# Performance work log

Hardware: AMD Instinct MI355X
Metric: run time of the kernel (lower is better)

Reference implementation:

```python
import jax, jax.numpy as jnp
import numpy as np

FILTERS = 128
DN = ('NHWC', 'HWIO', 'NHWC')
T1 = 1.0
RTOL = 1e-3
ATOL = 1e-3
DT0 = 0.05
MAX_STEPS = 32  # upper bound on adaptive solver steps (dopri5 at rtol=1e-3 uses far fewer)


def _conv(x, w):
    return jax.lax.conv_general_dilated(x, w, (1, 1), 'SAME', dimension_numbers=DN)


def _ode_func(y, t, w1, b1, w2, b2):
    # f(y, t) = relu(conv(relu(conv([y, t], w1)+b1) ++ t, w2)+b2), time appended as extra channel
    def cat_t(x):
        return jnp.concatenate([x, jnp.ones(x.shape[:-1] + (1,), x.dtype) * t], axis=-1)
    h = jax.nn.relu(_conv(cat_t(y), w1) + b1)
    return jax.nn.relu(_conv(cat_t(h), w2) + b2)


def _dopri5(y0, w1, b1, w2, b2):
    # Adaptive Dormand-Prince RK45 from t=0 to t=1, matching tf.contrib.integrate.odeint defaults
    f = lambda y, t: _ode_func(y, t, w1, b1, w2, b2)

    def rk_step(y, t, dt):
        k1 = f(y, t)
        k2 = f(y + dt * (0.2 * k1), t + 0.2 * dt)
        k3 = f(y + dt * (3. / 40 * k1 + 9. / 40 * k2), t + 0.3 * dt)
        k4 = f(y + dt * (44. / 45 * k1 - 56. / 15 * k2 + 32. / 9 * k3), t + 0.8 * dt)
        k5 = f(y + dt * (19372. / 6561 * k1 - 25360. / 2187 * k2 + 64448. / 6561 * k3
                         - 212. / 729 * k4), t + 8. / 9 * dt)
        k6 = f(y + dt * (9017. / 3168 * k1 - 355. / 33 * k2 + 46732. / 5247 * k3
                         + 49. / 176 * k4 - 5103. / 18656 * k5), t + dt)
        y5 = y + dt * (35. / 384 * k1 + 500. / 1113 * k3 + 125. / 192 * k4
                       - 2187. / 6784 * k5 + 11. / 84 * k6)
        k7 = f(y5, t + dt)  # FSAL stage, used only for the error estimate here
        err = dt * ((35. / 384 - 5179. / 57600) * k1 + (500. / 1113 - 7571. / 16695) * k3
                    + (125. / 192 - 393. / 640) * k4 + (-2187. / 6784 + 92097. / 339200) * k5
                    + (11. / 84 - 187. / 2100) * k6 - (1. / 40) * k7)
        return y5, err

    def step(carry, _):
        y, t, dt, done = carry
        dt_c = jnp.minimum(dt, T1 - t)  # never overshoot t1
        y_new, err = rk_step(y, t, dt_c)
        scale = ATOL + RTOL * jnp.maximum(jnp.abs(y), jnp.abs(y_new))
        err_norm = jnp.sqrt(jnp.mean(jnp.square(err / scale)))
        err_norm = jax.lax.stop_gradient(jnp.maximum(err_norm, 1e-10))
        accept = err_norm <= 1.0
        factor = jnp.clip(0.9 * err_norm ** -0.2, 0.2, 10.0)
        adv = accept & jnp.logical_not(done)
        y = jnp.where(adv, y_new, y)
        t = jnp.where(adv, t + dt_c, t)
        dt = jnp.where(done, dt, dt_c * factor)
        done = done | (t >= T1 - 1e-6)
        return (y, t, dt, done), None

    init = (y0, jnp.float32(0.0), jnp.float32(DT0), jnp.array(False))
    (y, _, _, _), _ = jax.lax.scan(jax.checkpoint(step), init, None, length=MAX_STEPS)
    return y


def setup_inputs() -> dict:
    key = jax.random.key(0)
    k0, k1, k2 = jax.random.split(key, 3)
    B, H, W, F = 32, 32, 32, FILTERS
    kh = kw = 3
    # glorot_uniform for HWIO conv kernel: fan_in = kh*kw*(F+1), fan_out = kh*kw*F
    lim = float(np.sqrt(6.0 / (kh * kw * (F + 1) + kh * kw * F)))
    x = jax.random.normal(k0, (B, H, W, F), jnp.float32)
    w1 = jax.random.uniform(k1, (kh, kw, F + 1, F), jnp.float32, -lim, lim)
    w2 = jax.random.uniform(k2, (kh, kw, F + 1, F), jnp.float32, -lim, lim)
    b1 = jnp.zeros((F,), jnp.float32)
    b2 = jnp.zeros((F,), jnp.float32)
    return {"x": x, "w1": w1, "b1": b1, "w2": w2, "b2": b2}


def reference(x, w1, b1, w2, b2):
    return _dopri5(x, w1, b1, w2, b2)
```

## Files before the change

kernel.cpp:

```cpp
#include <hip/hip_runtime.h>
#include <math.h>

#define NB    32
#define NHW   32
#define NC    128
#define NTOT  (NB*NHW*NHW*NC)
#define N4    (NTOT/4)
#define N8    (NTOT/8)
#define KDIM  1152

typedef unsigned short u16;
typedef __attribute__((ext_vector_type(8))) short short8v;
typedef __attribute__((ext_vector_type(4))) float float4v;

__device__ inline float b2f(u16 u) { union { unsigned int i; float f; } x; x.i = ((unsigned int)u) << 16; return x.f; }
__device__ inline u16   f2b(float f) {
    union { unsigned int i; float f; } x; x.f = f;
    unsigned int u = x.i;
    return (u16)((u + 0x7fffu + ((u >> 16) & 1u)) >> 16);
}
__device__ inline void ld8(const u16* __restrict__ p, float* v) {
    uint4 r = *(const uint4*)p;
    v[0] = b2f((u16)(r.x & 0xffff)); v[1] = b2f((u16)(r.x >> 16));
    v[2] = b2f((u16)(r.y & 0xffff)); v[3] = b2f((u16)(r.y >> 16));
    v[4] = b2f((u16)(r.z & 0xffff)); v[5] = b2f((u16)(r.z >> 16));
    v[6] = b2f((u16)(r.w & 0xffff)); v[7] = b2f((u16)(r.w >> 16));
}
__device__ inline uint4 pk8(const float* v) {
    uint4 o;
    o.x = (unsigned int)f2b(v[0]) | ((unsigned int)f2b(v[1]) << 16);
    o.y = (unsigned int)f2b(v[2]) | ((unsigned int)f2b(v[3]) << 16);
    o.z = (unsigned int)f2b(v[4]) | ((unsigned int)f2b(v[5]) << 16);
    o.w = (unsigned int)f2b(v[6]) | ((unsigned int)f2b(v[7]) << 16);
    return o;
}
__device__ inline void fma8(float* __restrict__ v, const u16* __restrict__ p, float s) {
    float kv[8];
    ld8(p, kv);
    #pragma unroll
    for (int j = 0; j < 8; ++j) v[j] = fmaf(s, kv[j], v[j]);
}


__global__ __launch_bounds__(64) void init_kernel(float* __restrict__ st, double* __restrict__ acc)
{
    int i = threadIdx.x;
    if (i < 32) acc[i] = 0.0;
    if (i == 0) { st[0]=0.0f; st[1]=0.05f; st[2]=0.05f; st[3]=0.0f; st[4]=0.0f; }
}

__global__ __launch_bounds__(256) void prep_kernel(
    const float* __restrict__ w, short* __restrict__ Wt, float* __restrict__ Et)
{
    const int part = blockIdx.x;
    const int tid = threadIdx.x;
    if (part < 9) {
        const int tap = part;
        for (int i = tid; i < 128*128; i += 256) {
            const int ci = i >> 7, co = i & 127;
            Wt[co*KDIM + tap*128 + ci] = (short)f2b(w[(tap*129 + ci)*128 + co]);
        }
    } else {
        for (int i = tid; i < 9*128; i += 256) {
            const int cls = i >> 7, co = i & 127;
            const int cy = cls / 3, cx = cls % 3;
            float s = 0.f;
            for (int ky = 0; ky < 3; ++ky) {
                if ((cy==0 && ky==0) || (cy==2 && ky==2)) continue;
                for (int kx = 0; kx < 3; ++kx) {
                    if ((cx==0 && kx==0) || (cx==2 && kx==2)) continue;
                    s += w[((ky*3+kx)*129 + 128)*128 + co];
                }
            }
            Et[cls*128 + co] = s;
        }
    }
}

__global__ __launch_bounds__(256) void copy_kernel(float* __restrict__ dst, const float* __restrict__ src)
{
    int stride = gridDim.x * blockDim.x;
    for (int i = blockIdx.x*blockDim.x + threadIdx.x; i < N4; i += stride)
        reinterpret_cast<float4*>(dst)[i] = reinterpret_cast<const float4*>(src)[i];
}

__global__ __launch_bounds__(256) void copy_if_adv_kernel(float* __restrict__ dst,
                                                          const float* __restrict__ src,
                                                          const float* __restrict__ st)
{
    if (st[4] == 0.0f) return;
    int stride = gridDim.x * blockDim.x;
    for (int i = blockIdx.x*blockDim.x + threadIdx.x; i < N4; i += stride)
        reinterpret_cast<float4*>(dst)[i] = reinterpret_cast<const float4*>(src)[i];
}

template<int NK>
__global__ __launch_bounds__(256) void conv_mfma(
    const float* __restrict__ basef, const u16* __restrict__ bfin,
    const u16* __restrict__ ka, const u16* __restrict__ kb,
    const u16* __restrict__ kc, const u16* __restrict__ kd,
    const u16* __restrict__ ke,
    float ca, float cb, float cc2, float cd, float ce,
    const short* __restrict__ Wt, const float* __restrict__ bias,
    const float* __restrict__ Et,
    u16* __restrict__ out,
    const float* __restrict__ st, float cfrac)
{
    if (st[3] != 0.0f) return;
    __shared__ __align__(16) char lds[180*256];
    const int b    = blockIdx.y;
    const int tile = blockIdx.x;
    const int ty   = (tile >> 2) * 16;
    const int tx   = (tile & 3) * 8;
    const int tid  = threadIdx.x;
    const float dt = st[2];

    const size_t ibase = (size_t)b * (NHW*NHW*NC);
    for (int i = tid; i < 180*16; i += 256) {
        const int pos = i >> 4, cc = i & 15;
        const int sy = pos / 10, sx = pos - sy*10;
        const int gy = ty + sy - 1, gx = tx + sx - 1;
        const bool ok = ((unsigned)gy < 32u) && ((unsigned)gx < 32u);
        uint4 w128;
        if (!ok) {
            w128 = make_uint4(0u, 0u, 0u, 0u);
        } else if (NK < 0) {
            w128 = *(const uint4*)(bfin + ibase + (size_t)(gy*32 + gx)*128 + cc*8);
        } else {
            const size_t idx = ibase + (size_t)(gy*32 + gx)*128 + cc*8;
            float v[8];
            *(float4*)(v)     = *(const float4*)(basef + idx);
            *(float4*)(v + 4) = *(const float4*)(basef + idx + 4);
            if (NK >= 1) fma8(v, ka + idx, dt*ca);
            if (NK >= 2) fma8(v, kb + idx, dt*cb);
            if (NK >= 3) fma8(v, kc + idx, dt*cc2);
            if (NK >= 4) fma8(v, kd + idx, dt*cd);
            if (NK >= 5) fma8(v, ke + idx, dt*ce);
            w128 = pk8(v);
        }
        *(uint4*)(lds + pos*256 + ((cc*16) ^ ((pos & 7) << 4))) = w128;
    }
    __syncthreads();

    const int l  = tid & 63;
    const int w  = tid >> 6;
    const int wy = w >> 1, wx = w & 1;
    const int lr = l & 15,  kg = l >> 4;

    float4v acc[4][4];
    #pragma unroll
    for (int ra = 0; ra < 4; ++ra)
        #pragma unroll
        for (int nb = 0; nb < 4; ++nb)
            acc[ra][nb] = (float4v){0.f, 0.f, 0.f, 0.f};

    int sy0[4], sx0[4];
    #pragma unroll
    for (int ra = 0; ra < 4; ++ra) {
        const int r = wy*64 + ra*16 + lr;
        sy0[ra] = r >> 3; sx0[ra] = r & 7;
    }

    #pragma unroll
    for (int ky = 0; ky < 3; ++ky) {
        #pragma unroll
        for (int kx = 0; kx < 3; ++kx) {
            const int tap = ky*3 + kx;
            #pragma unroll
            for (int kk = 0; kk < 4; ++kk) {
                short8v a[4], bb[4];
                const int cc = kk*4 + kg;
                #pragma unroll
                for (int ra = 0; ra < 4; ++ra) {
                    const int pos = (sy0[ra] + ky)*10 + sx0[ra] + kx;
                    a[ra] = *(const short8v*)(lds + pos*256 + ((cc*16) ^ ((pos & 7) << 4)));
                }
                const short* wb = Wt + tap*128 + kk*32 + kg*8;
                #pragma unroll
                for (int nb = 0; nb < 4; ++nb) {
                    const int cout = wx*64 + nb*16 + lr;
                    bb[nb] = *(const short8v*)(wb + (size_t)cout*KDIM);
                }
                #pragma unroll
                for (int ra = 0; ra < 4; ++ra)
                    #pragma unroll
                    for (int nb = 0; nb < 4; ++nb)
                        acc[ra][nb] = __builtin_amdgcn_mfma_f32_16x16x32_bf16(a[ra], bb[nb], acc[ra][nb], 0, 0, 0);
            }
        }
    }

    const float tval = st[0] + cfrac*dt;
    #pragma unroll
    for (int nb = 0; nb < 4; ++nb) {
        const int cout = wx*64 + nb*16 + lr;
        const float bsv = bias[cout];
        #pragma unroll
        for (int ra = 0; ra < 4; ++ra) {
            #pragma unroll
            for (int ri = 0; ri < 4; ++ri) {
                const int r  = wy*64 + ra*16 + kg*4 + ri;
                const int yy = ty + (r >> 3), xx = tx + (r & 7);
                const int cy = (yy == 0) ? 0 : ((yy == 31) ? 2 : 1);
                const int cx = (xx == 0) ? 0 : ((xx == 31) ? 2 : 1);
                float v = acc[ra][nb][ri] + bsv + tval*Et[(cy*3 + cx)*128 + cout];
                v = fmaxf(v, 0.f);
                out[(size_t)b*131072 + (size_t)(yy*32 + xx)*128 + cout] = f2b(v);
            }
        }
    }
}

__global__ __launch_bounds__(256) void axpy5_kernel(
    float* __restrict__ y5, const float* __restrict__ y,
    const u16* __restrict__ k1, const u16* __restrict__ k3,
    const u16* __restrict__ k4, const u16* __restrict__ k5,
    const u16* __restrict__ k6,
    float c1, float c3, float c4, float c5, float c6,
    const float* __restrict__ st)
{
    if (st[3] != 0.0f) return;
    const float dt = st[2];
    int stride = gridDim.x * blockDim.x;
    for (int i = blockIdx.x*blockDim.x + threadIdx.x; i < N8; i += stride) {
        const size_t base = (size_t)i * 8;
        float v[8];
        *(float4*)(v)     = *(const float4*)(y + base);
        *(float4*)(v + 4) = *(const float4*)(y + base + 4);
        fma8(v, k1 + base, dt*c1);
        fma8(v, k3 + base, dt*c3);
        fma8(v, k4 + base, dt*c4);
        fma8(v, k5 + base, dt*c5);
        fma8(v, k6 + base, dt*c6);
        *(float4*)(y5 + base)     = *(const float4*)(v);
        *(float4*)(y5 + base + 4) = *(const float4*)(v + 4);
    }
}

__global__ __launch_bounds__(256) void err_reduce_kernel(
    const float* __restrict__ y,  const float* __restrict__ y5,
    const u16* __restrict__ k1, const u16* __restrict__ k3,
    const u16* __restrict__ k4, const u16* __restrict__ k5,
    const u16* __restrict__ k6, const u16* __restrict__ k7,
    const float* __restrict__ st, double* __restrict__ acc_slot)
{
    if (st[3] != 0.0f) return;
    const float dt = st[2];
    const float E1 = (float)(35.0/384.0 - 5179.0/57600.0);
    const float E3 = (float)(500.0/1113.0 - 7571.0/16695.0);
    const float E4 = (float)(125.0/192.0 - 393.0/640.0);
    const float E5 = (float)(-2187.0/6784.0 + 92097.0/339200.0);
    const float E6 = (float)(11.0/84.0 - 187.0/2100.0);
    const float E7 = (float)(-1.0/40.0);
    float lsum = 0.f;
    int stride = gridDim.x*blockDim.x;
    for (int i = blockIdx.x*blockDim.x + threadIdx.x; i < N8; i += stride) {
        const size_t base = (size_t)i * 8;
        float a[8], c[8], d[8], e[8], f[8], g[8], yv[8], v5[8];
        ld8(k1 + base, a); ld8(k3 + base, c); ld8(k4 + base, d);
        ld8(k5 + base, e); ld8(k6 + base, f); ld8(k7 + base, g);
        *(float4*)(yv)     = *(const float4*)(y + base);
        *(float4*)(yv + 4) = *(const float4*)(y + base + 4);
        *(float4*)(v5)     = *(const float4*)(y5 + base);
        *(float4*)(v5 + 4) = *(const float4*)(y5 + base + 4);
        #pragma unroll
        for (int j = 0; j < 8; ++j) {
            float err = dt*(E1*a[j] + E3*c[j] + E4*d[j] + E5*e[j] + E6*f[j] + E7*g[j]);
            float sc  = 1e-3f + 1e-3f*fmaxf(fabsf(yv[j]), fabsf(v5[j]));
            float r = err/sc; lsum += r*r;
        }
    }
    #pragma unroll
    for (int off = 32; off > 0; off >>= 1) lsum += __shfl_down(lsum, off, 64);
    __shared__ float ws_[4];
    int wid = threadIdx.x >> 6, lane = threadIdx.x & 63;
    if (lane == 0) ws_[wid] = lsum;
    __syncthreads();
    if (threadIdx.x == 0) {
        float bs = ws_[0] + ws_[1] + ws_[2] + ws_[3];
        atomicAdd(acc_slot, (double)bs);
    }
}

__global__ __launch_bounds__(64) void ctrl_kernel(float* __restrict__ st, const double* __restrict__ acc_slot)
{
    if (threadIdx.x != 0) return;
    float t = st[0], dt = st[1], dtc = st[2];
    bool done = (st[3] != 0.0f);
    float err_norm = sqrtf((float)(*acc_slot / (double)NTOT));
    err_norm = fmaxf(err_norm, 1e-10f);
    bool accept = (err_norm <= 1.0f);
    float factor = 0.9f * powf(err_norm, -0.2f);
    factor = fminf(fmaxf(factor, 0.2f), 10.0f);
    bool adv = accept && !done;
    if (adv) t = t + dtc;
    if (!done) dt = dtc * factor;
    done = done || (t >= 1.0f - 1e-6f);
    st[0] = t; st[1] = dt; st[3] = done ? 1.0f : 0.0f; st[4] = adv ? 1.0f : 0.0f;
    st[2] = fminf(dt, 1.0f - t);
}

extern "C" void kernel_launch(void* const* d_in, const int* in_sizes, int n_in,
                              void* d_out, int out_size, void* d_ws, size_t ws_size,
                              hipStream_t stream)
{
    const float* x  = (const float*)d_in[0];
    const float* w1 = (const float*)d_in[1];
    const float* b1 = (const float*)d_in[2];
    const float* w2 = (const float*)d_in[3];
    const float* b2 = (const float*)d_in[4];

    char* ws = (char*)d_ws;
    double* acc = (double*)ws;
    float*  st  = (float*)(ws + 256);
    float*  E1t = (float*)(ws + 512);
    float*  E2t = (float*)(ws + 5120);
    short*  Wt1 = (short*)(ws + 10240);
    short*  Wt2 = (short*)(ws + 10240 + 294912);
    char*   bufs = ws + 1048576;
    float* y  = (float*)(bufs);
    float* y5 = (float*)(bufs + (size_t)NTOT*4);
    u16*   h  = (u16*)(bufs + (size_t)NTOT*8);
    u16*   k1 = (u16*)(bufs + (size_t)NTOT*10);
    u16*   k2 = (u16*)(bufs + (size_t)NTOT*12);
    u16*   k3 = (u16*)(bufs + (size_t)NTOT*14);
    u16*   k4 = (u16*)(bufs + (size_t)NTOT*16);
    u16*   k5 = (u16*)(bufs + (size_t)NTOT*18);
    u16*   k6 = (u16*)(bufs + (size_t)NTOT*20);
    u16*   k7 = (u16*)(bufs + (size_t)NTOT*22);

    const dim3 cgrid(8, NB);
    const dim3 cblk(256);
    const int ab = 2048;

    const float A21 = 0.2f;
    const float A31 = (float)(3.0/40.0),      A32 = (float)(9.0/40.0);
    const float A41 = (float)(44.0/45.0),     A42 = (float)(-56.0/15.0),     A43 = (float)(32.0/9.0);
    const float A51 = (float)(19372.0/6561.0),A52 = (float)(-25360.0/2187.0),A53 = (float)(64448.0/6561.0), A54 = (float)(-212.0/729.0);
    const float A61 = (float)(9017.0/3168.0), A62 = (float)(-355.0/33.0),    A63 = (float)(46732.0/5247.0), A64 = (float)(49.0/176.0), A65 = (float)(-5103.0/18656.0);
    const float B1  = (float)(35.0/384.0),    B3  = (float)(500.0/1113.0),   B4  = (float)(125.0/192.0),    B5  = (float)(-2187.0/6784.0), B6 = (float)(11.0/84.0);
    const float C2 = 0.2f, C3 = 0.3f, C4 = 0.8f, C5 = (float)(8.0/9.0);

    init_kernel<<<1, 64, 0, stream>>>(st, acc);
    prep_kernel<<<10, 256, 0, stream>>>(w1, Wt1, E1t);
    prep_kernel<<<10, 256, 0, stream>>>(w2, Wt2, E2t);
    copy_kernel<<<ab, 256, 0, stream>>>(y, x);

    for (int it = 0; it < 32; ++it) {
        conv_mfma<0><<<cgrid, cblk, 0, stream>>>(y, h, k1,k1,k1,k1,k1, 0,0,0,0,0, Wt1, b1, E1t, h,  st, 0.0f);
        conv_mfma<-1><<<cgrid, cblk, 0, stream>>>(y, h, k1,k1,k1,k1,k1, 0,0,0,0,0, Wt2, b2, E2t, k1, st, 0.0f);
        conv_mfma<1><<<cgrid, cblk, 0, stream>>>(y, h, k1,k1,k1,k1,k1, A21,0,0,0,0, Wt1, b1, E1t, h,  st, C2);
        conv_mfma<-1><<<cgrid, cblk, 0, stream>>>(y, h, k1,k1,k1,k1,k1, 0,0,0,0,0, Wt2, b2, E2t, k2, st, C2);
        conv_mfma<2><<<cgrid, cblk, 0, stream>>>(y, h, k1,k2,k1,k1,k1, A31,A32,0,0,0, Wt1, b1, E1t, h,  st, C3);
        conv_mfma<-1><<<cgrid, cblk, 0, stream>>>(y, h, k1,k1,k1,k1,k1, 0,0,0,0,0, Wt2, b2, E2t, k3, st, C3);
        conv_mfma<3><<<cgrid, cblk, 0, stream>>>(y, h, k1,k2,k3,k1,k1, A41,A42,A43,0,0, Wt1, b1, E1t, h,  st, C4);
        conv_mfma<-1><<<cgrid, cblk, 0, stream>>>(y, h, k1,k1,k1,k1,k1, 0,0,0,0,0, Wt2, b2, E2t, k4, st, C4);
        conv_mfma<4><<<cgrid, cblk, 0, stream>>>(y, h, k1,k2,k3,k4,k1, A51,A52,A53,A54,0, Wt1, b1, E1t, h,  st, C5);
        conv_mfma<-1><<<cgrid, cblk, 0, stream>>>(y, h, k1,k1,k1,k1,k1, 0,0,0,0,0, Wt2, b2, E2t, k5, st, C5);
        conv_mfma<5><<<cgrid, cblk, 0, stream>>>(y, h, k1,k2,k3,k4,k5, A61,A62,A63,A64,A65, Wt1, b1, E1t, h,  st, 1.0f);
        conv_mfma<-1><<<cgrid, cblk, 0, stream>>>(y, h, k1,k1,k1,k1,k1, 0,0,0,0,0, Wt2, b2, E2t, k6, st, 1.0f);
        axpy5_kernel<<<ab, 256, 0, stream>>>(y5, y, k1, k3, k4, k5, k6, B1, B3, B4, B5, B6, st);
        conv_mfma<0><<<cgrid, cblk, 0, stream>>>(y5, h, k1,k1,k1,k1,k1, 0,0,0,0,0, Wt1, b1, E1t, h,  st, 1.0f);
        conv_mfma<-1><<<cgrid, cblk, 0, stream>>>(y5, h, k1,k1,k1,k1,k1, 0,0,0,0,0, Wt2, b2, E2t, k7, st, 1.0f);
        err_reduce_kernel<<<ab, 256, 0, stream>>>(y, y5, k1, k3, k4, k5, k6, k7, st, acc + it);
        ctrl_kernel<<<1, 64, 0, stream>>>(st, acc + it);
        copy_if_adv_kernel<<<ab, 256, 0, stream>>>(y, y5, st);
    }

    copy_kernel<<<ab, 256, 0, stream>>>((float*)d_out, y);

    (void)in_sizes; (void)n_in; (void)out_size; (void)ws_size;
}
```

Before: 3.021 ms.

## Fuse whole adaptive ODE solve into one persistent cooperative kernel

Replaces the per-step chain of about eighteen kernel launches with a single cooperative persistent kernel that loops over solver steps using grid-wide syncs. Each RK stage fuses both convolutions, keeping the hidden activation in LDS with a halo-extended tile instead of writing it to global memory. The y5 combination is folded into the last stage, and the loop exits early once the integration reaches t=1. In exchange it recomputes halo pixels of the first conv, runs only 256 blocks of work per sync, and keeps the old multi-launch path as a fallback if the cooperative launch fails.

```diff
diff --git a/kernel.cpp b/kernel.cpp
--- a/kernel.cpp
+++ b/kernel.cpp
@@ -1,13 +1,16 @@
 #include <hip/hip_runtime.h>
+#include <hip/hip_cooperative_groups.h>
 #include <math.h>
 
-#define NB    32
-#define NHW   32
-#define NC    128
-#define NTOT  (NB*NHW*NHW*NC)
-#define N4    (NTOT/4)
-#define N8    (NTOT/8)
+namespace cg = cooperative_groups;
+
+#define NTOT  4194304
+#define N4    1048576
+#define N8    524288
 #define KDIM  1152
+#define GRID  256
+#define BLK   256
+#define NTH   (GRID*BLK)
 
 typedef unsigned short u16;
 typedef __attribute__((ext_vector_type(8))) short short8v;
@@ -39,6 +42,334 @@
     ld8(p, kv);
     #pragma unroll
     for (int j = 0; j < 8; ++j) v[j] = fmaf(s, kv[j], v[j]);
+}
+
+constexpr float A21 = 0.2f;
+constexpr float A31 = (float)(3.0/40.0),       A32 = (float)(9.0/40.0);
+constexpr float A41 = (float)(44.0/45.0),      A42 = (float)(-56.0/15.0),      A43 = (float)(32.0/9.0);
+constexpr float A51 = (float)(19372.0/6561.0), A52 = (float)(-25360.0/2187.0), A53 = (float)(64448.0/6561.0), A54 = (float)(-212.0/729.0);
+constexpr float A61 = (float)(9017.0/3168.0),  A62 = (float)(-355.0/33.0),     A63 = (float)(46732.0/5247.0), A64 = (float)(49.0/176.0), A65 = (float)(-5103.0/18656.0);
+constexpr float B1c = (float)(35.0/384.0),     B3c = (float)(500.0/1113.0),    B4c = (float)(125.0/192.0),    B5c = (float)(-2187.0/6784.0), B6c = (float)(11.0/84.0);
+constexpr float CF2 = 0.2f, CF3 = 0.3f, CF4 = 0.8f, CF5 = (float)(8.0/9.0);
+
+
+template<int NK, bool STY5>
+__device__ __forceinline__ void feval(
+    char* ldsA, char* ldsH,
+    const float* __restrict__ yb, float* __restrict__ y5b,
+    const u16* __restrict__ ka, const u16* __restrict__ kb,
+    const u16* __restrict__ kc, const u16* __restrict__ kd,
+    const u16* __restrict__ ke,
+    float ca, float cb, float cc, float cd, float ce,
+    const short* __restrict__ Wt1, const float* __restrict__ b1g, const float* __restrict__ E1g,
+    const short* __restrict__ Wt2, const float* __restrict__ b2g, const float* __restrict__ E2g,
+    u16* __restrict__ kout,
+    float tcur, float dt, float tfrac,
+    int img, int ty, int tx, int tid)
+{
+    const size_t ibase = (size_t)img * 131072;
+    const float tval = tcur + tfrac * dt;
+
+    {
+        const float s1 = dt*ca, s2 = dt*cb, s3 = dt*cc, s4 = dt*cd, s5 = dt*ce;
+        for (int i = tid; i < 144*16; i += BLK) {
+            const int pos = i >> 4, ch8 = i & 15;
+            const int iy = pos / 12, ix = pos - iy*12;
+            const int gy = ty + iy - 2, gx = tx + ix - 2;
+            uint4 w128 = make_uint4(0u, 0u, 0u, 0u);
+            if ((unsigned)gy < 32u && (unsigned)gx < 32u) {
+                const size_t idx = ibase + (size_t)((gy << 5) + gx)*128 + ch8*8;
+                float v[8];
+                *(float4*)(v)     = *(const float4*)(yb + idx);
+                *(float4*)(v + 4) = *(const float4*)(yb + idx + 4);
+                if (NK >= 1) fma8(v, ka + idx, s1);
+                if (NK >= 2) fma8(v, kb + idx, s2);
+                if (NK >= 3) fma8(v, kc + idx, s3);
+                if (NK >= 4) fma8(v, kd + idx, s4);
+                if (NK >= 5) fma8(v, ke + idx, s5);
+                if (STY5) {
+                    if ((unsigned)(iy - 2) < 8u && (unsigned)(ix - 2) < 8u) {
+                        *(float4*)(y5b + idx)     = *(const float4*)(v);
+                        *(float4*)(y5b + idx + 4) = *(const float4*)(v + 4);
+                    }
+                }
+                w128 = pk8(v);
+            }
+            *(uint4*)(ldsA + pos*256 + ((ch8*16) ^ ((pos & 7) << 4))) = w128;
+        }
+    }
+    __syncthreads();
+
+    const int l  = tid & 63, w = tid >> 6;
+    const int lr = l & 15,  kg = l >> 4;
+
+    {
+        float4v acc[2][8];
+        #pragma unroll
+        for (int j = 0; j < 2; ++j)
+            #pragma unroll
+            for (int cf = 0; cf < 8; ++cf) acc[j][cf] = (float4v){0.f, 0.f, 0.f, 0.f};
+        int py[2], px[2];
+        #pragma unroll
+        for (int j = 0; j < 2; ++j) {
+            const int p = (w*2 + j)*16 + lr;
+            py[j] = p / 10; px[j] = p - py[j]*10;
+        }
+        #pragma unroll 1
+        for (int ky = 0; ky < 3; ++ky) {
+            #pragma unroll 1
+            for (int kx = 0; kx < 3; ++kx) {
+                const int tap = ky*3 + kx;
+                #pragma unroll
+                for (int kk = 0; kk < 4; ++kk) {
+                    short8v a[2], bb[8];
+                    #pragma unroll
+                    for (int j = 0; j < 2; ++j) {
+                        int pp = (py[j] + ky)*12 + px[j] + kx;
+                        pp = (pp < 144) ? pp : 143;
+                        a[j] = *(const short8v*)(ldsA + pp*256 + ((16*(kk*4 + kg)) ^ ((pp & 7) << 4)));
+                    }
+                    const short* wb = Wt1 + tap*128 + kk*32 + kg*8;
+                    #pragma unroll
+                    for (int cf = 0; cf < 8; ++cf)
+                        bb[cf] = *(const short8v*)(wb + (size_t)(cf*16 + lr)*KDIM);
+                    #pragma unroll
+                    for (int j = 0; j < 2; ++j)
+                        #pragma unroll
+                        for (int cf = 0; cf < 8; ++cf)
+                            acc[j][cf] = __builtin_amdgcn_mfma_f32_16x16x32_bf16(a[j], bb[cf], acc[j][cf], 0, 0, 0);
+                }
+            }
+        }
+        int pA[2][4], ecls[2][4]; bool inA[2][4];
+        #pragma unroll
+        for (int j = 0; j < 2; ++j)
+            #pragma unroll
+            for (int ri = 0; ri < 4; ++ri) {
+                const int p = (w*2 + j)*16 + kg*4 + ri;
+                pA[j][ri] = p;
+                const int hy = p / 10, hx = p - (p/10)*10;
+                const int gy = ty + hy - 1, gx = tx + hx - 1;
+                inA[j][ri] = ((unsigned)gy < 32u) && ((unsigned)gx < 32u) && (p < 100);
+                const int cy = (gy == 0) ? 0 : ((gy == 31) ? 2 : 1);
+                const int cx = (gx == 0) ? 0 : ((gx == 31) ? 2 : 1);
+                ecls[j][ri] = (cy*3 + cx)*128;
+            }
+        #pragma unroll
+        for (int j = 0; j < 2; ++j)
+            #pragma unroll
+            for (int cf = 0; cf < 8; ++cf) {
+                const int c = cf*16 + lr;
+                const float bs = b1g[c];
+                #pragma unroll
+                for (int ri = 0; ri < 4; ++ri) {
+                    const int p = pA[j][ri];
+                    if (p < 100) {
+                        float v = 0.f;
+                        if (inA[j][ri]) v = fmaxf(acc[j][cf][ri] + bs + tval*E1g[ecls[j][ri] + c], 0.f);
+                        *(u16*)(ldsH + p*256 + ((2*c) ^ ((p & 7) << 4))) = f2b(v);
+                    }
+                }
+            }
+    }
+    __syncthreads();
+
+    {
+        float4v acc[8];
+        #pragma unroll
+        for (int cf = 0; cf < 8; ++cf) acc[cf] = (float4v){0.f, 0.f, 0.f, 0.f};
+        const int r = w*16 + lr;
+        const int oy = r >> 3, ox = r & 7;
+        #pragma unroll 1
+        for (int ky = 0; ky < 3; ++ky) {
+            #pragma unroll 1
+            for (int kx = 0; kx < 3; ++kx) {
+                const int tap = ky*3 + kx;
+                #pragma unroll
+                for (int kk = 0; kk < 4; ++kk) {
+                    const int p = (oy + ky)*10 + ox + kx;
+                    short8v a = *(const short8v*)(ldsH + p*256 + ((16*(kk*4 + kg)) ^ ((p & 7) << 4)));
+                    const short* wb = Wt2 + tap*128 + kk*32 + kg*8;
+                    short8v bb[8];
+                    #pragma unroll
+                    for (int cf = 0; cf < 8; ++cf)
+                        bb[cf] = *(const short8v*)(wb + (size_t)(cf*16 + lr)*KDIM);
+                    #pragma unroll
+                    for (int cf = 0; cf < 8; ++cf)
+                        acc[cf] = __builtin_amdgcn_mfma_f32_16x16x32_bf16(a, bb[cf], acc[cf], 0, 0, 0);
+                }
+            }
+        }
+        #pragma unroll
+        for (int ri = 0; ri < 4; ++ri) {
+            const int r2  = w*16 + kg*4 + ri;
+            const int gy  = ty + (r2 >> 3), gx = tx + (r2 & 7);
+            const int cy  = (gy == 0) ? 0 : ((gy == 31) ? 2 : 1);
+            const int cx  = (gx == 0) ? 0 : ((gx == 31) ? 2 : 1);
+            const int ecl = (cy*3 + cx)*128;
+            const size_t obase = ibase + (size_t)((gy << 5) + gx)*128;
+            #pragma unroll
+            for (int cf = 0; cf < 8; ++cf) {
+                const int c = cf*16 + lr;
+                float v = fmaxf(acc[cf][ri] + b2g[c] + tval*E2g[ecl + c], 0.f);
+                kout[obase + c] = f2b(v);
+            }
+        }
+    }
+}
+
+__device__ __forceinline__ void err_phase(
+    const float* __restrict__ y, const float* __restrict__ y5,
+    const u16* __restrict__ k1, const u16* __restrict__ k3,
+    const u16* __restrict__ k4, const u16* __restrict__ k5,
+    const u16* __restrict__ k6, const u16* __restrict__ k7,
+    float dt, double* __restrict__ slot, char* lds, int gtid, int tid)
+{
+    const float ER1 = (float)(35.0/384.0 - 5179.0/57600.0);
+    const float ER3 = (float)(500.0/1113.0 - 7571.0/16695.0);
+    const float ER4 = (float)(125.0/192.0 - 393.0/640.0);
+    const float ER5 = (float)(-2187.0/6784.0 + 92097.0/339200.0);
+    const float ER6 = (float)(11.0/84.0 - 187.0/2100.0);
+    const float ER7 = (float)(-1.0/40.0);
+    float lsum = 0.f;
+    for (int i = gtid; i < N8; i += NTH) {
+        const size_t base = (size_t)i * 8;
+        float a[8], c[8], d[8], e[8], f[8], g[8], yv[8], v5[8];
+        ld8(k1 + base, a); ld8(k3 + base, c); ld8(k4 + base, d);
+        ld8(k5 + base, e); ld8(k6 + base, f); ld8(k7 + base, g);
+        *(float4*)(yv)     = *(const float4*)(y + base);
+        *(float4*)(yv + 4) = *(const float4*)(y + base + 4);
+        *(float4*)(v5)     = *(const float4*)(y5 + base);
+        *(float4*)(v5 + 4) = *(const float4*)(y5 + base + 4);
+        #pragma unroll
+        for (int j = 0; j < 8; ++j) {
+            float err = dt*(ER1*a[j] + ER3*c[j] + ER4*d[j] + ER5*e[j] + ER6*f[j] + ER7*g[j]);
+            float sc  = 1e-3f + 1e-3f*fmaxf(fabsf(yv[j]), fabsf(v5[j]));
+            float rr = err/sc; lsum += rr*rr;
+        }
+    }
+    #pragma unroll
+    for (int off = 32; off > 0; off >>= 1) lsum += __shfl_down(lsum, off, 64);
+    float* ws4 = (float*)lds;
+    const int wid = tid >> 6, lane = tid & 63;
+    if (lane == 0) ws4[wid] = lsum;
+    __syncthreads();
+    if (tid == 0) atomicAdd(slot, (double)(ws4[0] + ws4[1] + ws4[2] + ws4[3]));
+    __syncthreads();
+}
+
+__device__ void ctrl_body(float* st, double a)
+{
+    float t = st[0], dt = st[1], dtc = st[2];
+    bool done = (st[3] != 0.0f);
+    float en = sqrtf((float)(a / (double)NTOT));
+    en = fmaxf(en, 1e-10f);
+    bool accept = (en <= 1.0f);
+    float factor = fminf(fmaxf(0.9f * powf(en, -0.2f), 0.2f), 10.0f);
+    bool adv = accept && !done;
+    if (adv) t += dtc;
+    if (!done) dt = dtc * factor;
+    done = done || (t >= 1.0f - 1e-6f);
+    st[0] = t; st[1] = dt; st[3] = done ? 1.0f : 0.0f; st[4] = adv ? 1.0f : 0.0f;
+    st[2] = fminf(dt, 1.0f - t);
+}
+
+#define DO_STAGE(NKv, STY5v, KA,KB,KC,KD,KE, CA,CB,CC,CD,CE, KOUT, TF)           \
+    _Pragma("unroll 1")                                                          \
+    for (int h2 = 0; h2 < 2; ++h2) {                                             \
+        const int wi  = bid + (h2 << 8);                                         \
+        feval<NKv,STY5v>(ldsA, ldsH, ycur, yalt, KA,KB,KC,KD,KE,                 \
+                         CA,CB,CC,CD,CE, Wt1,b1,E1t, Wt2,b2,E2t, KOUT,           \
+                         t, dt, TF, wi >> 4, ((wi >> 2) & 3)*8, (wi & 3)*8, tid);\
+    }                                                                            \
+    gg.sync();
+
+__global__ __launch_bounds__(BLK) void ode_persist(
+    const float* __restrict__ x,
+    const float* __restrict__ w1, const float* __restrict__ b1,
+    const float* __restrict__ w2, const float* __restrict__ b2,
+    char* __restrict__ ws, float* __restrict__ outp)
+{
+    __shared__ __align__(16) char ldsA[144*256];
+    __shared__ __align__(16) char ldsH[100*256];
+
+    cg::grid_group gg = cg::this_grid();
+
+    double* acc = (double*)ws;
+    float*  st  = (float*)(ws + 256);
+    float*  E1t = (float*)(ws + 512);
+    float*  E2t = (float*)(ws + 5120);
+    short*  Wt1 = (short*)(ws + 10240);
+    short*  Wt2 = (short*)(ws + 305152);
+    char*   bufs = ws + 1048576;
+    float* yA = (float*)(bufs);
+    float* yB = (float*)(bufs + (size_t)NTOT*4);
+    u16* k1 = (u16*)(bufs + (size_t)NTOT*8);
+    u16* k2 = (u16*)(bufs + (size_t)NTOT*10);
+    u16* k3 = (u16*)(bufs + (size_t)NTOT*12);
+    u16* k4 = (u16*)(bufs + (size_t)NTOT*14);
+    u16* k5 = (u16*)(bufs + (size_t)NTOT*16);
+    u16* k6 = (u16*)(bufs + (size_t)NTOT*18);
+    u16* k7 = (u16*)(bufs + (size_t)NTOT*20);
+
+    const int tid  = threadIdx.x;
+    const int bid  = blockIdx.x;
+    const int gtid = bid*BLK + tid;
+
+    for (int i = gtid; i < 9*128*128; i += NTH) {
+        const int tap = i >> 14, r = i & 16383;
+        const int ci = r >> 7, co = r & 127;
+        Wt1[co*KDIM + tap*128 + ci] = (short)f2b(w1[(tap*129 + ci)*128 + co]);
+        Wt2[co*KDIM + tap*128 + ci] = (short)f2b(w2[(tap*129 + ci)*128 + co]);
+    }
+    for (int i = gtid; i < 9*128; i += NTH) {
+        const int cls = i >> 7, co = i & 127;
+        const int cy = cls / 3, cx = cls - cy*3;
+        float s1 = 0.f, s2 = 0.f;
+        for (int ky = 0; ky < 3; ++ky) {
+            if ((cy == 0 && ky == 0) || (cy == 2 && ky == 2)) continue;
+            for (int kx = 0; kx < 3; ++kx) {
+                if ((cx == 0 && kx == 0) || (cx == 2 && kx == 2)) continue;
+                s1 += w1[((ky*3 + kx)*129 + 128)*128 + co];
+                s2 += w2[((ky*3 + kx)*129 + 128)*128 + co];
+            }
+        }
+        E1t[cls*128 + co] = s1;
+        E2t[cls*128 + co] = s2;
+    }
+    for (int i = gtid; i < N4; i += NTH)
+        ((float4*)yA)[i] = ((const float4*)x)[i];
+    if (gtid == 0) {
+        st[0] = 0.f; st[1] = 0.05f; st[2] = 0.05f; st[3] = 0.f; st[4] = 0.f;
+        for (int i = 0; i < 32; ++i) acc[i] = 0.0;
+    }
+    gg.sync();
+
+    float* ycur = yA;
+    float* yalt = yB;
+    volatile float* vst = st;
+
+    for (int it = 0; it < 32; ++it) {
+        if (vst[3] != 0.0f) break;
+        const float t = vst[0], dt = vst[2];
+
+        DO_STAGE(0,false, k1,k1,k1,k1,k1, 0,0,0,0,0,                  k1, 0.0f)
+        DO_STAGE(1,false, k1,k1,k1,k1,k1, A21,0,0,0,0,                k2, CF2)
+        DO_STAGE(2,false, k1,k2,k2,k2,k2, A31,A32,0,0,0,              k3, CF3)
+        DO_STAGE(3,false, k1,k2,k3,k3,k3, A41,A42,A43,0,0,            k4, CF4)
+        DO_STAGE(4,false, k1,k2,k3,k4,k4, A51,A52,A53,A54,0,          k5, CF5)
+        DO_STAGE(5,false, k1,k2,k3,k4,k5, A61,A62,A63,A64,A65,        k6, 1.0f)
+        DO_STAGE(5,true,  k1,k3,k4,k5,k6, B1c,B3c,B4c,B5c,B6c,        k7, 1.0f)
+
+        err_phase(ycur, yalt, k1, k3, k4, k5, k6, k7, dt, acc + it, ldsA, gtid, tid);
+        gg.sync();
+        if (gtid == 0) ctrl_body(st, acc[it]);
+        gg.sync();
+        if (vst[4] != 0.0f) { float* tmp = ycur; ycur = yalt; yalt = tmp; }
+    }
+
+    for (int i = gtid; i < N4; i += NTH)
+        ((float4*)outp)[i] = ((const float4*)ycur)[i];
 }
 
 
@@ -115,7 +446,7 @@
     const int tid  = threadIdx.x;
     const float dt = st[2];
 
-    const size_t ibase = (size_t)b * (NHW*NHW*NC);
+    const size_t ibase = (size_t)b * 131072;
     for (int i = tid; i < 180*16; i += 256) {
         const int pos = i >> 4, cc = i & 15;
         const int sy = pos / 10, sx = pos - sy*10;
@@ -246,12 +577,12 @@
 {
     if (st[3] != 0.0f) return;
     const float dt = st[2];
-    const float E1 = (float)(35.0/384.0 - 5179.0/57600.0);
-    const float E3 = (float)(500.0/1113.0 - 7571.0/16695.0);
-    const float E4 = (float)(125.0/192.0 - 393.0/640.0);
-    const float E5 = (float)(-2187.0/6784.0 + 92097.0/339200.0);
-    const float E6 = (float)(11.0/84.0 - 187.0/2100.0);
-    const float E7 = (float)(-1.0/40.0);
+    const float ER1 = (float)(35.0/384.0 - 5179.0/57600.0);
+    const float ER3 = (float)(500.0/1113.0 - 7571.0/16695.0);
+    const float ER4 = (float)(125.0/192.0 - 393.0/640.0);
+    const float ER5 = (float)(-2187.0/6784.0 + 92097.0/339200.0);
+    const float ER6 = (float)(11.0/84.0 - 187.0/2100.0);
+    const float ER7 = (float)(-1.0/40.0);
     float lsum = 0.f;
     int stride = gridDim.x*blockDim.x;
     for (int i = blockIdx.x*blockDim.x + threadIdx.x; i < N8; i += stride) {
@@ -265,9 +596,9 @@
         *(float4*)(v5 + 4) = *(const float4*)(y5 + base + 4);
         #pragma unroll
         for (int j = 0; j < 8; ++j) {
-            float err = dt*(E1*a[j] + E3*c[j] + E4*d[j] + E5*e[j] + E6*f[j] + E7*g[j]);
+            float err = dt*(ER1*a[j] + ER3*c[j] + ER4*d[j] + ER5*e[j] + ER6*f[j] + ER7*g[j]);
             float sc  = 1e-3f + 1e-3f*fmaxf(fabsf(yv[j]), fabsf(v5[j]));
-            float r = err/sc; lsum += r*r;
+            float rr = err/sc; lsum += rr*rr;
         }
     }
     #pragma unroll
@@ -285,89 +616,89 @@
 __global__ __launch_bounds__(64) void ctrl_kernel(float* __restrict__ st, const double* __restrict__ acc_slot)
 {
     if (threadIdx.x != 0) return;
-    float t = st[0], dt = st[1], dtc = st[2];
-    bool done = (st[3] != 0.0f);
-    float err_norm = sqrtf((float)(*acc_slot / (double)NTOT));
-    err_norm = fmaxf(err_norm, 1e-10f);
-    bool accept = (err_norm <= 1.0f);
-    float factor = 0.9f * powf(err_norm, -0.2f);
-    factor = fminf(fmaxf(factor, 0.2f), 10.0f);
-    bool adv = accept && !done;
-    if (adv) t = t + dtc;
-    if (!done) dt = dtc * factor;
-    done = done || (t >= 1.0f - 1e-6f);
-    st[0] = t; st[1] = dt; st[3] = done ? 1.0f : 0.0f; st[4] = adv ? 1.0f : 0.0f;
-    st[2] = fminf(dt, 1.0f - t);
-}
+    ctrl_body(st, *acc_slot);
+}
+
 
 extern "C" void kernel_launch(void* const* d_in, const int* in_sizes, int n_in,
                               void* d_out, int out_size, void* d_ws, size_t ws_size,
                               hipStream_t stream)
 {
-    const float* x  = (const float*)d_in[0];
-    const float* w1 = (const float*)d_in[1];
-    const float* b1 = (const float*)d_in[2];
-    const float* w2 = (const float*)d_in[3];
-    const float* b2 = (const float*)d_in[4];
-
-    char* ws = (char*)d_ws;
-    double* acc = (double*)ws;
-    float*  st  = (float*)(ws + 256);
-    float*  E1t = (float*)(ws + 512);
-    float*  E2t = (float*)(ws + 5120);
-    short*  Wt1 = (short*)(ws + 10240);
-    short*  Wt2 = (short*)(ws + 10240 + 294912);
-    char*   bufs = ws + 1048576;
+    const float* xp  = (const float*)d_in[0];
+    const float* w1p = (const float*)d_in[1];
+    const float* b1p = (const float*)d_in[2];
+    const float* w2p = (const float*)d_in[3];
+    const float* b2p = (const float*)d_in[4];
+    char*  wsp  = (char*)d_ws;
+    float* outp = (float*)d_out;
+
+    void* kargs[7];
+    kargs[0] = (void*)&xp;
+    kargs[1] = (void*)&w1p;
+    kargs[2] = (void*)&b1p;
+    kargs[3] = (void*)&w2p;
+    kargs[4] = (void*)&b2p;
+    kargs[5] = (void*)&wsp;
+    kargs[6] = (void*)&outp;
+
+    hipError_t rc = hipLaunchCooperativeKernel((const void*)ode_persist,
+                                               dim3(GRID), dim3(BLK),
+                                               kargs, 0, stream);
+    if (rc == hipSuccess) {
+        (void)in_sizes; (void)n_in; (void)out_size; (void)ws_size;
+        return;
+    }
+    (void)hipGetLastError();
+
+    double* acc = (double*)wsp;
+    float*  st  = (float*)(wsp + 256);
+    float*  E1t = (float*)(wsp + 512);
+    float*  E2t = (float*)(wsp + 5120);
+    short*  Wt1 = (short*)(wsp + 10240);
+    short*  Wt2 = (short*)(wsp + 305152);
+    char*   bufs = wsp + 1048576;
     float* y  = (float*)(bufs);
     float* y5 = (float*)(bufs + (size_t)NTOT*4);
-    u16*   h  = (u16*)(bufs + (size_t)NTOT*8);
-    u16*   k1 = (u16*)(bufs + (size_t)NTOT*10);
-    u16*   k2 = (u16*)(bufs + (size_t)NTOT*12);
-    u16*   k3 = (u16*)(bufs + (size_t)NTOT*14);
-    u16*   k4 = (u16*)(bufs + (size_t)NTOT*16);
-    u16*   k5 = (u16*)(bufs + (size_t)NTOT*18);
-    u16*   k6 = (u16*)(bufs + (size_t)NTOT*20);
-    u16*   k7 = (u16*)(bufs + (size_t)NTOT*22);
-
-    const dim3 cgrid(8, NB);
+    u16* k1 = (u16*)(bufs + (size_t)NTOT*8);
+    u16* k2 = (u16*)(bufs + (size_t)NTOT*10);
+    u16* k3 = (u16*)(bufs + (size_t)NTOT*12);
+    u16* k4 = (u16*)(bufs + (size_t)NTOT*14);
+    u16* k5 = (u16*)(bufs + (size_t)NTOT*16);
+    u16* k6 = (u16*)(bufs + (size_t)NTOT*18);
+    u16* k7 = (u16*)(bufs + (size_t)NTOT*20);
+    u16* h  = (u16*)(bufs + (size_t)NTOT*22);
+
+    const dim3 cgrid(8, 32);
     const dim3 cblk(256);
     const int ab = 2048;
 
-    const float A21 = 0.2f;
-    const float A31 = (float)(3.0/40.0),      A32 = (float)(9.0/40.0);
-    const float A41 = (float)(44.0/45.0),     A42 = (float)(-56.0/15.0),     A43 = (float)(32.0/9.0);
-    const float A51 = (float)(19372.0/6561.0),A52 = (float)(-25360.0/2187.0),A53 = (float)(64448.0/6561.0), A54 = (float)(-212.0/729.0);
-    const float A61 = (float)(9017.0/3168.0), A62 = (float)(-355.0/33.0),    A63 = (float)(46732.0/5247.0), A64 = (float)(49.0/176.0), A65 = (float)(-5103.0/18656.0);
-    const float B1  = (float)(35.0/384.0),    B3  = (float)(500.0/1113.0),   B4  = (float)(125.0/192.0),    B5  = (float)(-2187.0/6784.0), B6 = (float)(11.0/84.0);
-    const float C2 = 0.2f, C3 = 0.3f, C4 = 0.8f, C5 = (float)(8.0/9.0);
-
     init_kernel<<<1, 64, 0, stream>>>(st, acc);
-    prep_kernel<<<10, 256, 0, stream>>>(w1, Wt1, E1t);
-    prep_kernel<<<10, 256, 0, stream>>>(w2, Wt2, E2t);
-    copy_kernel<<<ab, 256, 0, stream>>>(y, x);
+    prep_kernel<<<10, 256, 0, stream>>>(w1p, Wt1, E1t);
+    prep_kernel<<<10, 256, 0, stream>>>(w2p, Wt2, E2t);
+    copy_kernel<<<ab, 256, 0, stream>>>(y, xp);
 
     for (int it = 0; it < 32; ++it) {
-        conv_mfma<0><<<cgrid, cblk, 0, stream>>>(y, h, k1,k1,k1,k1,k1, 0,0,0,0,0, Wt1, b1, E1t, h,  st, 0.0f);
-        conv_mfma<-1><<<cgrid, cblk, 0, stream>>>(y, h, k1,k1,k1,k1,k1, 0,0,0,0,0, Wt2, b2, E2t, k1, st, 0.0f);
-        conv_mfma<1><<<cgrid, cblk, 0, stream>>>(y, h, k1,k1,k1,k1,k1, A21,0,0,0,0, Wt1, b1, E1t, h,  st, C2);
-        conv_mfma<-1><<<cgrid, cblk, 0, stream>>>(y, h, k1,k1,k1,k1,k1, 0,0,0,0,0, Wt2, b2, E2t, k2, st, C2);
-        conv_mfma<2><<<cgrid, cblk, 0, stream>>>(y, h, k1,k2,k1,k1,k1, A31,A32,0,0,0, Wt1, b1, E1t, h,  st, C3);
-        conv_mfma<-1><<<cgrid, cblk, 0, stream>>>(y, h, k1,k1,k1,k1,k1, 0,0,0,0,0, Wt2, b2, E2t, k3, st, C3);
-        conv_mfma<3><<<cgrid, cblk, 0, stream>>>(y, h, k1,k2,k3,k1,k1, A41,A42,A43,0,0, Wt1, b1, E1t, h,  st, C4);
-        conv_mfma<-1><<<cgrid, cblk, 0, stream>>>(y, h, k1,k1,k1,k1,k1, 0,0,0,0,0, Wt2, b2, E2t, k4, st, C4);
-        conv_mfma<4><<<cgrid, cblk, 0, stream>>>(y, h, k1,k2,k3,k4,k1, A51,A52,A53,A54,0, Wt1, b1, E1t, h,  st, C5);
-        conv_mfma<-1><<<cgrid, cblk, 0, stream>>>(y, h, k1,k1,k1,k1,k1, 0,0,0,0,0, Wt2, b2, E2t, k5, st, C5);
-        conv_mfma<5><<<cgrid, cblk, 0, stream>>>(y, h, k1,k2,k3,k4,k5, A61,A62,A63,A64,A65, Wt1, b1, E1t, h,  st, 1.0f);
-        conv_mfma<-1><<<cgrid, cblk, 0, stream>>>(y, h, k1,k1,k1,k1,k1, 0,0,0,0,0, Wt2, b2, E2t, k6, st, 1.0f);
-        axpy5_kernel<<<ab, 256, 0, stream>>>(y5, y, k1, k3, k4, k5, k6, B1, B3, B4, B5, B6, st);
-        conv_mfma<0><<<cgrid, cblk, 0, stream>>>(y5, h, k1,k1,k1,k1,k1, 0,0,0,0,0, Wt1, b1, E1t, h,  st, 1.0f);
-        conv_mfma<-1><<<cgrid, cblk, 0, stream>>>(y5, h, k1,k1,k1,k1,k1, 0,0,0,0,0, Wt2, b2, E2t, k7, st, 1.0f);
+        conv_mfma<0><<<cgrid, cblk, 0, stream>>>(y, h, k1,k1,k1,k1,k1, 0,0,0,0,0, Wt1, b1p, E1t, h,  st, 0.0f);
+        conv_mfma<-1><<<cgrid, cblk, 0, stream>>>(y, h, k1,k1,k1,k1,k1, 0,0,0,0,0, Wt2, b2p, E2t, k1, st, 0.0f);
+        conv_mfma<1><<<cgrid, cblk, 0, stream>>>(y, h, k1,k1,k1,k1,k1, A21,0,0,0,0, Wt1, b1p, E1t, h,  st, CF2);
+        conv_mfma<-1><<<cgrid, cblk, 0, stream>>>(y, h, k1,k1,k1,k1,k1, 0,0,0,0,0, Wt2, b2p, E2t, k2, st, CF2);
+        conv_mfma<2><<<cgrid, cblk, 0, stream>>>(y, h, k1,k2,k1,k1,k1, A31,A32,0,0,0, Wt1, b1p, E1t, h,  st, CF3);
+        conv_mfma<-1><<<cgrid, cblk, 0, stream>>>(y, h, k1,k1,k1,k1,k1, 0,0,0,0,0, Wt2, b2p, E2t, k3, st, CF3);
+        conv_mfma<3><<<cgrid, cblk, 0, stream>>>(y, h, k1,k2,k3,k1,k1, A41,A42,A43,0,0, Wt1, b1p, E1t, h,  st, CF4);
+        conv_mfma<-1><<<cgrid, cblk, 0, stream>>>(y, h, k1,k1,k1,k1,k1, 0,0,0,0,0, Wt2, b2p, E2t, k4, st, CF4);
+        conv_mfma<4><<<cgrid, cblk, 0, stream>>>(y, h, k1,k2,k3,k4,k1, A51,A52,A53,A54,0, Wt1, b1p, E1t, h,  st, CF5);
+        conv_mfma<-1><<<cgrid, cblk, 0, stream>>>(y, h, k1,k1,k1,k1,k1, 0,0,0,0,0, Wt2, b2p, E2t, k5, st, CF5);
+        conv_mfma<5><<<cgrid, cblk, 0, stream>>>(y, h, k1,k2,k3,k4,k5, A61,A62,A63,A64,A65, Wt1, b1p, E1t, h,  st, 1.0f);
+        conv_mfma<-1><<<cgrid, cblk, 0, stream>>>(y, h, k1,k1,k1,k1,k1, 0,0,0,0,0, Wt2, b2p, E2t, k6, st, 1.0f);
+        axpy5_kernel<<<ab, 256, 0, stream>>>(y5, y, k1, k3, k4, k5, k6, B1c, B3c, B4c, B5c, B6c, st);
+        conv_mfma<0><<<cgrid, cblk, 0, stream>>>(y5, h, k1,k1,k1,k1,k1, 0,0,0,0,0, Wt1, b1p, E1t, h,  st, 1.0f);
+        conv_mfma<-1><<<cgrid, cblk, 0, stream>>>(y5, h, k1,k1,k1,k1,k1, 0,0,0,0,0, Wt2, b2p, E2t, k7, st, 1.0f);
         err_reduce_kernel<<<ab, 256, 0, stream>>>(y, y5, k1, k3, k4, k5, k6, k7, st, acc + it);
         ctrl_kernel<<<1, 64, 0, stream>>>(st, acc + it);
         copy_if_adv_kernel<<<ab, 256, 0, stream>>>(y, y5, st);
     }
 
-    copy_kernel<<<ab, 256, 0, stream>>>((float*)d_out, y);
+    copy_kernel<<<ab, 256, 0, stream>>>(outp, y);
 
     (void)in_sizes; (void)n_in; (void)out_size; (void)ws_size;
 }
```

New measurement: 6.557 ms. 117% more time.
